# Performance work log

Hardware: AMD Instinct MI355X
Metric: run time of the kernel (lower is better)

The kernel has to match this reference:

```python
import jax, jax.numpy as jnp
import numpy as np

B, T, C, H = 32, 2048, 1024, 64


def setup_inputs() -> dict:
    key = jax.random.key(0)
    k1, k2, k3, k4 = jax.random.split(key, 4)
    x = jax.random.normal(k1, (B, T, C), dtype=jnp.float32)
    # nn.Linear(C, H, bias=False) weights, stored here as [C, H] for x @ W
    s = 1.0 / np.sqrt(C)
    Wk = jax.random.uniform(k2, (C, H), jnp.float32, -s, s)
    Wq = jax.random.uniform(k3, (C, H), jnp.float32, -s, s)
    Wv = jax.random.uniform(k4, (C, H), jnp.float32, -s, s)
    return {"x": x, "Wk": Wk, "Wq": Wq, "Wv": Wv}


def reference(x, Wk, Wq, Wv):
    # projections: [B,T,C] @ [C,H] -> [B,T,H]
    k = jnp.einsum('btc,ch->bth', x, Wk)
    q = jnp.einsum('btc,ch->bth', x, Wq)
    v = jnp.einsum('btc,ch->bth', x, Wv)
    Hd = k.shape[-1]
    # attention scores [B,T,T], scaled by head_size^-0.5
    scores = jnp.einsum('bqh,bkh->bqk', q, k) * (Hd ** -0.5)
    # causal mask: masked_fill where triu(ones, 1)==1 -> -inf (mask strict upper triangle)
    Tq = x.shape[1]
    causal = jnp.tril(jnp.ones((Tq, Tq), dtype=bool))  # True = keep
    scores = jnp.where(causal, scores, -jnp.inf)
    attn = jax.nn.softmax(scores, axis=-1)
    # dropout: identity in eval/reference mode
    out = jnp.einsum('bqk,bkh->bqh', attn, v)
    return out
```

## Files before the change

kernel.cpp:

```cpp
#include <hip/hip_runtime.h>
#include <hip/hip_bf16.h>

typedef short bf16x8 __attribute__((ext_vector_type(8)));
typedef float f32x4 __attribute__((ext_vector_type(4)));

#define B_ 32
#define T_ 2048
#define C_ 1024
#define H_ 64

__device__ __forceinline__ ushort f2bf(float f) {
  union { float f; unsigned u; } v; v.f = f;
  unsigned u = v.u;
  return (ushort)((u + 0x7FFFu + ((u >> 16) & 1u)) >> 16);
}

__device__ __forceinline__ bf16x8 pack8(float4 a, float4 b) {
  union { __hip_bfloat162 h; short2 s; } t;
  bf16x8 r;
  t.h = __float22bfloat162_rn(make_float2(a.x, a.y)); r[0] = t.s.x; r[1] = t.s.y;
  t.h = __float22bfloat162_rn(make_float2(a.z, a.w)); r[2] = t.s.x; r[3] = t.s.y;
  t.h = __float22bfloat162_rn(make_float2(b.x, b.y)); r[4] = t.s.x; r[5] = t.s.y;
  t.h = __float22bfloat162_rn(make_float2(b.z, b.w)); r[6] = t.s.x; r[7] = t.s.y;
  return r;
}

__device__ __forceinline__ void async_copy16(void* lds, const void* g) {
  __builtin_amdgcn_global_load_lds(
      (const __attribute__((address_space(1))) unsigned int*)g,
      (__attribute__((address_space(3))) unsigned int*)lds, 16, 0, 0);
}

__global__ __launch_bounds__(256) void wconv_kernel(
    const float* __restrict__ Wk, const float* __restrict__ Wq,
    const float* __restrict__ Wv, ushort* __restrict__ Wt) {
  int idx = blockIdx.x * 256 + threadIdx.x;
  if (idx >= 3 * 64 * C_) return;
  int n = idx >> 10, c = idx & 1023;
  int mat = n >> 6, h = n & 63;
  const float* W = (mat == 0) ? Wk : (mat == 1 ? Wq : Wv);
  float v = W[c * 64 + h];
  if (mat == 1) v *= 0.18033688011112042f;
  Wt[idx] = f2bf(v);
}

__global__ __launch_bounds__(256, 4) void qkv_kernel(
    const float* __restrict__ x, const ushort* __restrict__ Wt,
    ushort* __restrict__ Kb, ushort* __restrict__ Qb, ushort* __restrict__ Vt) {
  __shared__ __align__(16) ushort Bs[192 * 64];
  int tid = threadIdx.x;
  int wave = tid >> 6, lane = tid & 63, quad = lane >> 4, l16 = lane & 15;
  int r0 = blockIdx.x * 64;
  const float* xr = x + (size_t)(r0 + wave * 16 + l16) * C_;

  f32x4 acc[12];
#pragma unroll
  for (int nt = 0; nt < 12; ++nt) acc[nt] = (f32x4){0.f, 0.f, 0.f, 0.f};

  for (int k0 = 0; k0 < C_; k0 += 64) {
    __syncthreads();
#pragma unroll
    for (int i = 0; i < 6; ++i) {
      int id = tid + 256 * i;
      int n = id >> 3, p = id & 7, c = p ^ (n & 7);
      async_copy16((char*)Bs + id * 16, Wt + (size_t)n * C_ + k0 + c * 8);
    }
    float4 a0 = *(const float4*)(xr + k0 + quad * 8);
    float4 a1 = *(const float4*)(xr + k0 + quad * 8 + 4);
    float4 a2 = *(const float4*)(xr + k0 + 32 + quad * 8);
    float4 a3 = *(const float4*)(xr + k0 + 32 + quad * 8 + 4);
    __syncthreads();

    bf16x8 af0 = pack8(a0, a1);
    bf16x8 af1 = pack8(a2, a3);
#pragma unroll
    for (int nt = 0; nt < 12; ++nt) {
      int n = nt * 16 + l16;
      bf16x8 b0 = *(const bf16x8*)(Bs + n * 64 + ((quad ^ (l16 & 7)) << 3));
      bf16x8 b1 = *(const bf16x8*)(Bs + n * 64 + (((4 + quad) ^ (l16 & 7)) << 3));
      acc[nt] = __builtin_amdgcn_mfma_f32_16x16x32_bf16(af0, b0, acc[nt], 0, 0, 0);
      acc[nt] = __builtin_amdgcn_mfma_f32_16x16x32_bf16(af1, b1, acc[nt], 0, 0, 0);
    }
  }

  int b = r0 >> 11;
  int rowbase = r0 + wave * 16 + quad * 4;
#pragma unroll
  for (int nt = 0; nt < 12; ++nt) {
    int mat = nt >> 2;
    int h = (nt & 3) * 16 + l16;
    if (mat == 2) {
      ushort4 pv;
      pv.x = f2bf(acc[nt][0]); pv.y = f2bf(acc[nt][1]);
      pv.z = f2bf(acc[nt][2]); pv.w = f2bf(acc[nt][3]);
      *(ushort4*)(&Vt[(size_t)b * H_ * T_ + (size_t)h * T_ + (rowbase & (T_ - 1))]) = pv;
    } else {
      ushort* dst = (mat == 0) ? Kb : Qb;
#pragma unroll
      for (int r = 0; r < 4; ++r)
        dst[(size_t)(rowbase + r) * H_ + h] = f2bf(acc[nt][r]);
    }
  }
}

__global__ __launch_bounds__(256, 2) void attn_kernel(
    const ushort* __restrict__ Qb, const ushort* __restrict__ Kb,
    const ushort* __restrict__ Vt, float* __restrict__ out) {
  __shared__ __align__(16) ushort Ks[2][128 * 64];
  __shared__ __align__(16) ushort Vs[2][64 * 128];
  __shared__ __align__(16) ushort Pl[4][16 * 128];

  int tid = threadIdx.x;
  int wave = tid >> 6, lane = tid & 63, quad = lane >> 4, l16 = lane & 15;
  int bid = blockIdx.x;
  int xcd = bid & 7, wi = bid >> 3;
  int batch = xcd * 4 + (wi & 3);
  int spair = wi >> 2;
  const ushort* Qbase = Qb + (size_t)batch * T_ * H_;
  const ushort* Kbase = Kb + (size_t)batch * T_ * H_;
  const ushort* Vbase = Vt + (size_t)batch * H_ * T_;
  ushort* Pw = &Pl[wave][0];

  auto stage = [&](int jc, int buf) {
    int j0 = jc * 128;
#pragma unroll
    for (int g = 0; g < 4; ++g) {
      int id = tid + 256 * g;
      int n = id >> 3, p = id & 7, c = p ^ (n & 7);
      async_copy16((char*)&Ks[buf][0] + id * 16,
                   Kbase + (size_t)(j0 + n) * H_ + c * 8);
    }
#pragma unroll
    for (int g = 0; g < 4; ++g) {
      int id = tid + 256 * g;
      int r = id >> 4, p = id & 15, c = p ^ (r & 15);
      async_copy16((char*)&Vs[buf][0] + id * 16,
                   Vbase + (size_t)r * T_ + j0 + c * 8);
    }
  };

#pragma unroll 1
  for (int half = 0; half < 2; ++half) {
    int qseg = half ? spair : 31 - spair;
    int q0 = qseg * 64 + wave * 16;
    const ushort* qr = Qbase + (size_t)(q0 + l16) * H_;
    bf16x8 qf0 = *(const bf16x8*)(qr + quad * 8);
    bf16x8 qf1 = *(const bf16x8*)(qr + 32 + quad * 8);

    f32x4 o[4];
    float m_i[4], l_i[4];
#pragma unroll
    for (int i = 0; i < 4; ++i) {
      o[i] = (f32x4){0.f, 0.f, 0.f, 0.f};
      m_i[i] = -1e30f; l_i[i] = 0.f;
    }

    int nch = (qseg >> 1) + 1;
    __syncthreads();
    stage(0, 0);
    int cur = 0;
#pragma unroll 1
    for (int jc = 0; jc < nch; ++jc, cur ^= 1) {
      int j0 = jc * 128;
      __syncthreads();
      if (jc + 1 < nch) stage(jc + 1, cur ^ 1);
      const ushort* KsC = &Ks[cur][0];
      const ushort* VsC = &Vs[cur][0];

      f32x4 sv[8];
      __builtin_amdgcn_s_setprio(1);
#pragma unroll
      for (int nt = 0; nt < 8; ++nt) {
        int n = nt * 16 + l16;
        bf16x8 kf0 = *(const bf16x8*)(KsC + n * 64 + ((quad ^ (l16 & 7)) << 3));
        bf16x8 kf1 = *(const bf16x8*)(KsC + n * 64 + (((4 + quad) ^ (l16 & 7)) << 3));
        f32x4 z = (f32x4){0.f, 0.f, 0.f, 0.f};
        z = __builtin_amdgcn_mfma_f32_16x16x32_bf16(qf0, kf0, z, 0, 0, 0);
        z = __builtin_amdgcn_mfma_f32_16x16x32_bf16(qf1, kf1, z, 0, 0, 0);
        sv[nt] = z;
      }
      __builtin_amdgcn_s_setprio(0);

      if (jc == nch - 1) {
        int rowg = q0 + quad * 4;
#pragma unroll
        for (int nt = 0; nt < 8; ++nt) {
          int col = j0 + nt * 16 + l16;
#pragma unroll
          for (int rr = 0; rr < 4; ++rr)
            if (col > rowg + rr) sv[nt][rr] = -1e30f;
        }
      }

      float pm[4];
#pragma unroll
      for (int rr = 0; rr < 4; ++rr) {
        float v = fmaxf(fmaxf(fmaxf(sv[0][rr], sv[1][rr]), fmaxf(sv[2][rr], sv[3][rr])),
                        fmaxf(fmaxf(sv[4][rr], sv[5][rr]), fmaxf(sv[6][rr], sv[7][rr])));
        v = fmaxf(v, __shfl_xor(v, 1));
        v = fmaxf(v, __shfl_xor(v, 2));
        v = fmaxf(v, __shfl_xor(v, 4));
        v = fmaxf(v, __shfl_xor(v, 8));
        pm[rr] = v;
      }
      bool grow = (pm[0] > m_i[0] + 8.f) || (pm[1] > m_i[1] + 8.f) ||
                  (pm[2] > m_i[2] + 8.f) || (pm[3] > m_i[3] + 8.f);
      if (__any(grow)) {
#pragma unroll
        for (int rr = 0; rr < 4; ++rr) {
          float mn = fmaxf(m_i[rr], pm[rr]);
          float alpha = exp2f(m_i[rr] - mn);
          m_i[rr] = mn;
          l_i[rr] *= alpha;
#pragma unroll
          for (int ht = 0; ht < 4; ++ht) o[ht][rr] *= alpha;
        }
      }

      float rsum[4] = {0.f, 0.f, 0.f, 0.f};
#pragma unroll
      for (int nt = 0; nt < 8; ++nt)
#pragma unroll
        for (int rr = 0; rr < 4; ++rr) {
          float p = exp2f(sv[nt][rr] - m_i[rr]);
          rsum[rr] += p;
          int row = quad * 4 + rr;
          int swz = (nt * 2 + (l16 >> 3)) ^ row;
          Pw[row * 128 + (swz << 3) + (l16 & 7)] = f2bf(p);
        }
#pragma unroll
      for (int rr = 0; rr < 4; ++rr) l_i[rr] += rsum[rr];

      bf16x8 pf[4];
#pragma unroll
      for (int k = 0; k < 4; ++k)
        pf[k] = *(const bf16x8*)(&Pw[l16 * 128 + (((quad + 4 * k) ^ l16) << 3)]);
      __builtin_amdgcn_s_setprio(1);
#pragma unroll
      for (int ht = 0; ht < 4; ++ht) {
        int hrow = ht * 16 + l16;
#pragma unroll
        for (int k = 0; k < 4; ++k) {
          bf16x8 vf = *(const bf16x8*)(VsC + hrow * 128 + (((4 * k + quad) ^ l16) << 3));
          o[ht] = __builtin_amdgcn_mfma_f32_16x16x32_bf16(pf[k], vf, o[ht], 0, 0, 0);
        }
      }
      __builtin_amdgcn_s_setprio(0);
    }

#pragma unroll
    for (int rr = 0; rr < 4; ++rr) {
      float v = l_i[rr];
      v += __shfl_xor(v, 1);
      v += __shfl_xor(v, 2);
      v += __shfl_xor(v, 4);
      v += __shfl_xor(v, 8);
      l_i[rr] = __builtin_amdgcn_rcpf(v);
    }
    int rowbase = q0 + quad * 4;
#pragma unroll
    for (int ht = 0; ht < 4; ++ht)
#pragma unroll
      for (int rr = 0; rr < 4; ++rr)
        out[((size_t)batch * T_ + rowbase + rr) * H_ + ht * 16 + l16] =
            o[ht][rr] * l_i[rr];
  }
}

extern "C" void kernel_launch(void* const* d_in, const int* in_sizes, int n_in,
                              void* d_out, int out_size, void* d_ws, size_t ws_size,
                              hipStream_t stream) {
  const float* x  = (const float*)d_in[0];
  const float* Wk = (const float*)d_in[1];
  const float* Wq = (const float*)d_in[2];
  const float* Wv = (const float*)d_in[3];
  float* out = (float*)d_out;

  ushort* Wt = (ushort*)d_ws;
  ushort* Kb = (ushort*)((char*)d_ws + (1 << 19));
  ushort* Qb = Kb + (size_t)B_ * T_ * H_;
  ushort* Vt = Qb + (size_t)B_ * T_ * H_;

  hipLaunchKernelGGL(wconv_kernel, dim3(768), dim3(256), 0, stream, Wk, Wq, Wv, Wt);
  hipLaunchKernelGGL(qkv_kernel, dim3(1024), dim3(256), 0, stream, x, Wt, Kb, Qb, Vt);
  hipLaunchKernelGGL(attn_kernel, dim3(512), dim3(256), 0, stream, Qb, Kb, Vt, out);
}
```

Measured before the change: 435.2 us.

## Compute transposed scores to keep P in registers and prefetch x in QKV

The attention kernel now computes S^T = K·Q^T, so each lane holds one query row's probabilities. Those are packed to bf16 in registers and fed straight into 16x16x16 MFMAs against V, removing the per-wave LDS round trip for P. The row max and sum reductions drop from four shuffles per row to two, and the output is written as float4. The QKV projection also software-prefetches the next x slice before the MFMA loop. The trade-off is twice as many smaller MFMAs for the PV product and extra live registers for the prefetch.

Result: no change. 436.1 us (+0.2%).

```diff
diff --git a/kernel.cpp b/kernel.cpp
--- a/kernel.cpp
+++ b/kernel.cpp
@@ -2,6 +2,7 @@
 #include <hip/hip_bf16.h>
 
 typedef short bf16x8 __attribute__((ext_vector_type(8)));
+typedef short bf16x4 __attribute__((ext_vector_type(4)));
 typedef float f32x4 __attribute__((ext_vector_type(4)));
 
 #define B_ 32
@@ -9,10 +10,33 @@
 #define C_ 1024
 #define H_ 64
 
+#if defined(__HIP_DEVICE_COMPILE__)
+#if __has_builtin(__builtin_amdgcn_mfma_f32_16x16x16bf16_1k)
+#define MFMA16(A, Bo, Co) __builtin_amdgcn_mfma_f32_16x16x16bf16_1k(A, Bo, Co, 0, 0, 0)
+#elif __has_builtin(__builtin_amdgcn_mfma_f32_16x16x16_bf16)
+#define MFMA16(A, Bo, Co) __builtin_amdgcn_mfma_f32_16x16x16_bf16(A, Bo, Co, 0, 0, 0)
+#else
+static __device__ __forceinline__ f32x4 mfma16_asm(bf16x4 a, bf16x4 b, f32x4 c) {
+  f32x4 d;
+  asm("v_mfma_f32_16x16x16_bf16 %0, %1, %2, %3" : "=v"(d) : "v"(a), "v"(b), "v"(c));
+  return d;
+}
+#define MFMA16(A, Bo, Co) mfma16_asm(A, Bo, Co)
+#endif
+#else
+#define MFMA16(A, Bo, Co) (Co)
+#endif
+
 __device__ __forceinline__ ushort f2bf(float f) {
   union { float f; unsigned u; } v; v.f = f;
   unsigned u = v.u;
   return (ushort)((u + 0x7FFFu + ((u >> 16) & 1u)) >> 16);
+}
+
+__device__ __forceinline__ unsigned cvt_pk_bf16(float lo, float hi) {
+  unsigned r;
+  asm("v_cvt_pk_bf16_f32 %0, %1, %2" : "=v"(r) : "v"(lo), "v"(hi));
+  return r;
 }
 
 __device__ __forceinline__ bf16x8 pack8(float4 a, float4 b) {
@@ -57,6 +81,11 @@
 #pragma unroll
   for (int nt = 0; nt < 12; ++nt) acc[nt] = (f32x4){0.f, 0.f, 0.f, 0.f};
 
+  float4 a0 = *(const float4*)(xr + quad * 8);
+  float4 a1 = *(const float4*)(xr + quad * 8 + 4);
+  float4 a2 = *(const float4*)(xr + 32 + quad * 8);
+  float4 a3 = *(const float4*)(xr + 32 + quad * 8 + 4);
+
   for (int k0 = 0; k0 < C_; k0 += 64) {
     __syncthreads();
 #pragma unroll
@@ -65,11 +94,15 @@
       int n = id >> 3, p = id & 7, c = p ^ (n & 7);
       async_copy16((char*)Bs + id * 16, Wt + (size_t)n * C_ + k0 + c * 8);
     }
-    float4 a0 = *(const float4*)(xr + k0 + quad * 8);
-    float4 a1 = *(const float4*)(xr + k0 + quad * 8 + 4);
-    float4 a2 = *(const float4*)(xr + k0 + 32 + quad * 8);
-    float4 a3 = *(const float4*)(xr + k0 + 32 + quad * 8 + 4);
     __syncthreads();
+
+    float4 n0 = a0, n1 = a1, n2 = a2, n3 = a3;
+    if (k0 + 64 < C_) {
+      n0 = *(const float4*)(xr + k0 + 64 + quad * 8);
+      n1 = *(const float4*)(xr + k0 + 64 + quad * 8 + 4);
+      n2 = *(const float4*)(xr + k0 + 96 + quad * 8);
+      n3 = *(const float4*)(xr + k0 + 96 + quad * 8 + 4);
+    }
 
     bf16x8 af0 = pack8(a0, a1);
     bf16x8 af1 = pack8(a2, a3);
@@ -81,6 +114,7 @@
       acc[nt] = __builtin_amdgcn_mfma_f32_16x16x32_bf16(af0, b0, acc[nt], 0, 0, 0);
       acc[nt] = __builtin_amdgcn_mfma_f32_16x16x32_bf16(af1, b1, acc[nt], 0, 0, 0);
     }
+    a0 = n0; a1 = n1; a2 = n2; a3 = n3;
   }
 
   int b = r0 >> 11;
@@ -108,7 +142,6 @@
     const ushort* __restrict__ Vt, float* __restrict__ out) {
   __shared__ __align__(16) ushort Ks[2][128 * 64];
   __shared__ __align__(16) ushort Vs[2][64 * 128];
-  __shared__ __align__(16) ushort Pl[4][16 * 128];
 
   int tid = threadIdx.x;
   int wave = tid >> 6, lane = tid & 63, quad = lane >> 4, l16 = lane & 15;
@@ -119,7 +152,6 @@
   const ushort* Qbase = Qb + (size_t)batch * T_ * H_;
   const ushort* Kbase = Kb + (size_t)batch * T_ * H_;
   const ushort* Vbase = Vt + (size_t)batch * H_ * T_;
-  ushort* Pw = &Pl[wave][0];
 
   auto stage = [&](int jc, int buf) {
     int j0 = jc * 128;
@@ -148,12 +180,9 @@
     bf16x8 qf1 = *(const bf16x8*)(qr + 32 + quad * 8);
 
     f32x4 o[4];
-    float m_i[4], l_i[4];
-#pragma unroll
-    for (int i = 0; i < 4; ++i) {
-      o[i] = (f32x4){0.f, 0.f, 0.f, 0.f};
-      m_i[i] = -1e30f; l_i[i] = 0.f;
-    }
+#pragma unroll
+    for (int i = 0; i < 4; ++i) o[i] = (f32x4){0.f, 0.f, 0.f, 0.f};
+    float m_i = -1e30f, l_i = 0.f;
 
     int nch = (qseg >> 1) + 1;
     __syncthreads();
@@ -175,95 +204,84 @@
         bf16x8 kf0 = *(const bf16x8*)(KsC + n * 64 + ((quad ^ (l16 & 7)) << 3));
         bf16x8 kf1 = *(const bf16x8*)(KsC + n * 64 + (((4 + quad) ^ (l16 & 7)) << 3));
         f32x4 z = (f32x4){0.f, 0.f, 0.f, 0.f};
-        z = __builtin_amdgcn_mfma_f32_16x16x32_bf16(qf0, kf0, z, 0, 0, 0);
-        z = __builtin_amdgcn_mfma_f32_16x16x32_bf16(qf1, kf1, z, 0, 0, 0);
+        z = __builtin_amdgcn_mfma_f32_16x16x32_bf16(kf0, qf0, z, 0, 0, 0);
+        z = __builtin_amdgcn_mfma_f32_16x16x32_bf16(kf1, qf1, z, 0, 0, 0);
         sv[nt] = z;
       }
       __builtin_amdgcn_s_setprio(0);
 
       if (jc == nch - 1) {
-        int rowg = q0 + quad * 4;
+        int qg = q0 + l16;
 #pragma unroll
         for (int nt = 0; nt < 8; ++nt) {
-          int col = j0 + nt * 16 + l16;
+          int jb = j0 + nt * 16 + quad * 4;
 #pragma unroll
           for (int rr = 0; rr < 4; ++rr)
-            if (col > rowg + rr) sv[nt][rr] = -1e30f;
+            if (jb + rr > qg) sv[nt][rr] = -1e30f;
         }
       }
 
-      float pm[4];
-#pragma unroll
-      for (int rr = 0; rr < 4; ++rr) {
-        float v = fmaxf(fmaxf(fmaxf(sv[0][rr], sv[1][rr]), fmaxf(sv[2][rr], sv[3][rr])),
-                        fmaxf(fmaxf(sv[4][rr], sv[5][rr]), fmaxf(sv[6][rr], sv[7][rr])));
-        v = fmaxf(v, __shfl_xor(v, 1));
-        v = fmaxf(v, __shfl_xor(v, 2));
-        v = fmaxf(v, __shfl_xor(v, 4));
-        v = fmaxf(v, __shfl_xor(v, 8));
-        pm[rr] = v;
-      }
-      bool grow = (pm[0] > m_i[0] + 8.f) || (pm[1] > m_i[1] + 8.f) ||
-                  (pm[2] > m_i[2] + 8.f) || (pm[3] > m_i[3] + 8.f);
-      if (__any(grow)) {
-#pragma unroll
-        for (int rr = 0; rr < 4; ++rr) {
-          float mn = fmaxf(m_i[rr], pm[rr]);
-          float alpha = exp2f(m_i[rr] - mn);
-          m_i[rr] = mn;
-          l_i[rr] *= alpha;
-#pragma unroll
-          for (int ht = 0; ht < 4; ++ht) o[ht][rr] *= alpha;
+      float t8[8];
+#pragma unroll
+      for (int nt = 0; nt < 8; ++nt)
+        t8[nt] = fmaxf(fmaxf(sv[nt][0], sv[nt][1]), fmaxf(sv[nt][2], sv[nt][3]));
+      float pm = fmaxf(fmaxf(fmaxf(t8[0], t8[1]), fmaxf(t8[2], t8[3])),
+                       fmaxf(fmaxf(t8[4], t8[5]), fmaxf(t8[6], t8[7])));
+      pm = fmaxf(pm, __shfl_xor(pm, 16));
+      pm = fmaxf(pm, __shfl_xor(pm, 32));
+
+      if (__any(pm > m_i + 8.f)) {
+        float mn = fmaxf(m_i, pm);
+        float alpha = exp2f(m_i - mn);
+        m_i = mn; l_i *= alpha;
+#pragma unroll
+        for (int ht = 0; ht < 4; ++ht)
+#pragma unroll
+          for (int rr = 0; rr < 4; ++rr) o[ht][rr] *= alpha;
+      }
+
+      unsigned pk[8][2];
+      float rs = 0.f;
+#pragma unroll
+      for (int nt = 0; nt < 8; ++nt) {
+        float p0 = exp2f(sv[nt][0] - m_i);
+        float p1 = exp2f(sv[nt][1] - m_i);
+        float p2 = exp2f(sv[nt][2] - m_i);
+        float p3 = exp2f(sv[nt][3] - m_i);
+        rs += (p0 + p1) + (p2 + p3);
+        pk[nt][0] = cvt_pk_bf16(p0, p1);
+        pk[nt][1] = cvt_pk_bf16(p2, p3);
+      }
+      l_i += rs;
+
+      __builtin_amdgcn_s_setprio(1);
+#pragma unroll
+      for (int ht = 0; ht < 4; ++ht) {
+        int rowb = (ht * 16 + l16) * 128;
+#pragma unroll
+        for (int nt = 0; nt < 8; ++nt) {
+          int chk = (nt * 2 + (quad >> 1)) ^ l16;
+          bf16x4 vf = *(const bf16x4*)(VsC + rowb + (chk << 3) + ((quad & 1) << 2));
+          union { unsigned u[2]; bf16x4 v; } pb;
+          pb.u[0] = pk[nt][0]; pb.u[1] = pk[nt][1];
+          o[ht] = MFMA16(vf, pb.v, o[ht]);
         }
       }
-
-      float rsum[4] = {0.f, 0.f, 0.f, 0.f};
-#pragma unroll
-      for (int nt = 0; nt < 8; ++nt)
-#pragma unroll
-        for (int rr = 0; rr < 4; ++rr) {
-          float p = exp2f(sv[nt][rr] - m_i[rr]);
-          rsum[rr] += p;
-          int row = quad * 4 + rr;
-          int swz = (nt * 2 + (l16 >> 3)) ^ row;
-          Pw[row * 128 + (swz << 3) + (l16 & 7)] = f2bf(p);
-        }
-#pragma unroll
-      for (int rr = 0; rr < 4; ++rr) l_i[rr] += rsum[rr];
-
-      bf16x8 pf[4];
-#pragma unroll
-      for (int k = 0; k < 4; ++k)
-        pf[k] = *(const bf16x8*)(&Pw[l16 * 128 + (((quad + 4 * k) ^ l16) << 3)]);
-      __builtin_amdgcn_s_setprio(1);
-#pragma unroll
-      for (int ht = 0; ht < 4; ++ht) {
-        int hrow = ht * 16 + l16;
-#pragma unroll
-        for (int k = 0; k < 4; ++k) {
-          bf16x8 vf = *(const bf16x8*)(VsC + hrow * 128 + (((4 * k + quad) ^ l16) << 3));
-          o[ht] = __builtin_amdgcn_mfma_f32_16x16x32_bf16(pf[k], vf, o[ht], 0, 0, 0);
-        }
-      }
       __builtin_amdgcn_s_setprio(0);
     }
 
-#pragma unroll
-    for (int rr = 0; rr < 4; ++rr) {
-      float v = l_i[rr];
-      v += __shfl_xor(v, 1);
-      v += __shfl_xor(v, 2);
-      v += __shfl_xor(v, 4);
-      v += __shfl_xor(v, 8);
-      l_i[rr] = __builtin_amdgcn_rcpf(v);
-    }
-    int rowbase = q0 + quad * 4;
-#pragma unroll
-    for (int ht = 0; ht < 4; ++ht)
-#pragma unroll
-      for (int rr = 0; rr < 4; ++rr)
-        out[((size_t)batch * T_ + rowbase + rr) * H_ + ht * 16 + l16] =
-            o[ht][rr] * l_i[rr];
+    float ls = l_i;
+    ls += __shfl_xor(ls, 16);
+    ls += __shfl_xor(ls, 32);
+    float linv = __builtin_amdgcn_rcpf(ls);
+    float* orow = out + ((size_t)batch * T_ + q0 + l16) * H_;
+#pragma unroll
+    for (int ht = 0; ht < 4; ++ht) {
+      float4 st;
+      st.x = o[ht][0] * linv; st.y = o[ht][1] * linv;
+      st.z = o[ht][2] * linv; st.w = o[ht][3] * linv;
+      *(float4*)(orow + ht * 16 + quad * 4) = st;
+    }
   }
 }
 
```
